# Kernel tuning notes

Hardware: AMD Instinct MI355X
Metric: run time of the kernel (lower is better)

## Reference

```python
import jax, jax.numpy as jnp
import numpy as np

N_NODES = 100000
N_EDGES = 1600000
N_GRAPHS = 64
N_TYPES = 17   # len(TYPES)
D = 128        # embedding_dim == hidden_dim
H = 128
O = 128


def setup_inputs() -> dict:
    key = jax.random.key(0)
    ks = jax.random.split(key, 8)
    node_ids = jax.random.randint(ks[0], (N_NODES,), 0, N_TYPES)
    edge_index = jax.random.randint(ks[1], (2, N_EDGES), 0, N_NODES)
    batch = jnp.sort(jax.random.randint(ks[2], (N_NODES,), 0, N_GRAPHS))
    emb_table = jax.random.normal(ks[3], (N_TYPES, D), dtype=jnp.float32)
    W1 = jax.random.normal(ks[4], (D, H), dtype=jnp.float32) * (1.0 / np.sqrt(D))
    b1 = jnp.zeros((H,), dtype=jnp.float32)
    W2 = jax.random.normal(ks[5], (H, O), dtype=jnp.float32) * (1.0 / np.sqrt(H))
    b2 = jnp.zeros((O,), dtype=jnp.float32)
    return {"node_ids": node_ids, "edge_index": edge_index, "batch": batch,
            "num_graphs": N_GRAPHS, "emb_table": emb_table,
            "W1": W1, "b1": b1, "W2": W2, "b2": b2}


def _gcn_conv(x, W, b, src, dst, n_nodes):
    # PyG GCNConv: h = x W; symmetric norm with self-loops (src/dst already include them);
    # out[i] = sum_{e: dst_e=i} norm_e * h[src_e] + b
    h = x @ W
    deg = jax.ops.segment_sum(jnp.ones_like(dst, dtype=h.dtype), dst,
                              num_segments=n_nodes)
    dinv = jnp.where(deg > 0, jax.lax.rsqrt(deg), 0.0)
    norm = dinv[src] * dinv[dst]                      # [E+N]
    msgs = h[src] * norm[:, None]                     # [E+N, out_dim]
    return jax.ops.segment_sum(msgs, dst, num_segments=n_nodes) + b


def reference(node_ids, edge_index, batch, num_graphs, emb_table, W1, b1, W2, b2):
    n = node_ids.shape[0]
    loops = jnp.arange(n, dtype=edge_index.dtype)
    src = jnp.concatenate([edge_index[0], loops])
    dst = jnp.concatenate([edge_index[1], loops])

    x = emb_table[node_ids]                            # embedding lookup [N, D]
    x = _gcn_conv(x, W1, b1, src, dst, n)
    x = jax.nn.relu(x)
    # F.dropout(training=self.training) is identity in eval mode
    x = _gcn_conv(x, W2, b2, src, dst, n)

    # global_mean_pool over batch index
    sums = jax.ops.segment_sum(x, batch, num_segments=num_graphs)   # [G, O]
    cnts = jax.ops.segment_sum(jnp.ones((n,), dtype=x.dtype), batch,
                               num_segments=num_graphs)
    return sums / jnp.maximum(cnts, 1.0)[:, None]
```

## Files before the change

### kernel.cpp

```cpp
#include <hip/hip_runtime.h>
#include <hip/hip_bf16.h>


#define DDIM 128
#define GMAX 64
#define BPG  8
#define NBK  (GMAX * BPG)
#define BKCAP 4096
#define CHUNK 2048
#define MAXGN 2048
typedef unsigned int uint;
typedef unsigned short ushort;
typedef float v2f __attribute__((ext_vector_type(2)));

__global__ void __launch_bounds__(256) k_setup(
        const int* __restrict__ batch, int N,
        int* __restrict__ gBound, int* __restrict__ bkBound,
        const float* __restrict__ emb, const float* __restrict__ W1,
        float* __restrict__ t1) {
    int t = threadIdx.x, b = blockIdx.x;
    if (b == 0) {
        __shared__ int gB[GMAX + 1];
        if (t <= GMAX) {
            int key = t, lo = 0, hi = N;
            while (lo < hi) {
                int mid = (lo + hi) >> 1;
                if (batch[mid] < key) lo = mid + 1; else hi = mid;
            }
            gB[t] = lo;
            gBound[t] = lo;
        }
        __syncthreads();
        for (int bk = t; bk <= NBK; bk += 256) {
            int v;
            if (bk == NBK) v = gB[GMAX];
            else {
                int g = bk >> 3, s = bk & 7;
                int A = gB[g], L = gB[g + 1] - A;
                v = A + (int)(((long long)L * s + 7) / 8);
            }
            bkBound[bk] = v;
        }
    } else {
        int row = b - 1;
        if (t < DDIM) {
            float acc = 0.f;
            for (int k = 0; k < DDIM; k++) acc += emb[row * DDIM + k] * W1[k * DDIM + t];
            t1[row * DDIM + t] = acc;
        }
    }
}

__global__ void __launch_bounds__(256) k_ninfo(
        const int* __restrict__ batch, const int* __restrict__ gBound,
        uint* __restrict__ nodeInfo, int N) {
    int n = blockIdx.x * 256 + threadIdx.x;
    if (n >= N) return;
    int g = batch[n];
    int A = gBound[g], L = gBound[g + 1] - A;
    int o = n - A;
    int s = (8 * o) / L;
    nodeInfo[n] = ((uint)(g * BPG + s) << 12) | (uint)o;
}

__global__ void __launch_bounds__(256) k_partA(
        const int* __restrict__ src, const int* __restrict__ dst,
        const uint* __restrict__ nodeInfo, int* __restrict__ bkCnt,
        uint* __restrict__ partsKey, int E) {
    __shared__ int rk[NBK];
    __shared__ int runOff[NBK];
    __shared__ int base[NBK];
    __shared__ int sms[256];
    __shared__ uint sbuf[CHUNK];
    __shared__ ushort sb2[CHUNK];
    int t = threadIdx.x, b = blockIdx.x;
    int lo = b * CHUNK;
    int hi = lo + CHUNK; if (hi > E) hi = E;
    int cnt = hi - lo;
    for (int k = t; k < NBK; k += 256) rk[k] = 0;
    __syncthreads();
    uint key_[8]; int bk_[8], r_[8]; bool v_[8];
    if (cnt == CHUNK) {
        int4 sA = *(const int4*)(src + lo + t * 4);
        int4 sB = *(const int4*)(src + lo + 1024 + t * 4);
        int4 dA = *(const int4*)(dst + lo + t * 4);
        int4 dB = *(const int4*)(dst + lo + 1024 + t * 4);
        int ss[8] = {sA.x, sA.y, sA.z, sA.w, sB.x, sB.y, sB.z, sB.w};
        int dd[8] = {dA.x, dA.y, dA.z, dA.w, dB.x, dB.y, dB.z, dB.w};
#pragma unroll
        for (int q = 0; q < 8; q++) {
            v_[q] = true;
            uint info = nodeInfo[dd[q]];
            bk_[q] = (int)(info >> 12);
            key_[q] = ((info & 0xFFFu) << 17) | (uint)ss[q];
        }
    } else {
#pragma unroll
        for (int q = 0; q < 8; q++) {
            int item = lo + q * 256 + t;
            v_[q] = item < hi;
            key_[q] = 0; bk_[q] = 0;
            if (v_[q]) {
                uint info = nodeInfo[dst[item]];
                bk_[q] = (int)(info >> 12);
                key_[q] = ((info & 0xFFFu) << 17) | (uint)src[item];
            }
        }
    }
#pragma unroll
    for (int q = 0; q < 8; q++)
        if (v_[q]) r_[q] = atomicAdd(&rk[bk_[q]], 1);
    __syncthreads();
    {
        int v0 = rk[2 * t], v1 = rk[2 * t + 1];
        int run = v0 + v1;
        sms[t] = run; __syncthreads();
        for (int off = 1; off < 256; off <<= 1) {
            int a = (t >= off) ? sms[t - off] : 0;
            __syncthreads();
            sms[t] += a; __syncthreads();
        }
        int excl = sms[t] - run;
        runOff[2 * t] = excl;
        runOff[2 * t + 1] = excl + v0;
    }
    __syncthreads();
    for (int k = t; k < NBK; k += 256) {
        int c = rk[k];
        if (c > 0) base[k] = k * BKCAP + atomicAdd(&bkCnt[k], c);
    }
#pragma unroll
    for (int q = 0; q < 8; q++)
        if (v_[q]) {
            int p = runOff[bk_[q]] + r_[q];
            sbuf[p] = key_[q];
            sb2[p] = (ushort)bk_[q];
        }
    __syncthreads();
#pragma unroll
    for (int q = 0; q < 8; q++) {
        int p = q * 256 + t;
        if (p < cnt) {
            int bk = sb2[p];
            partsKey[base[bk] + (p - runOff[bk])] = sbuf[p];
        }
    }
}

__global__ void __launch_bounds__(256) k_cnt2(
        const uint* __restrict__ partsKey, const int* __restrict__ bkBound,
        const int* __restrict__ bkCnt, const int* __restrict__ ids,
        float2* __restrict__ nd, float* __restrict__ dinvA) {
    __shared__ int cnt[256];
    int b = blockIdx.x, t = threadIdx.x;
    cnt[t] = 0;
    __syncthreads();
    int nodeLo = bkBound[b];
    int gOff = nodeLo - bkBound[(b >> 3) << 3];
    int lo = b * BKCAP, hi = lo + bkCnt[b];
    for (int idx = lo + t; idx < hi; idx += 256) {
        uint key = partsKey[idx];
        int dL = (int)((key >> 17) & 0xFFF) - gOff;
        atomicAdd(&cnt[dL], 1);
    }
    __syncthreads();
    int nn = bkBound[b + 1] - nodeLo;
    if (t < nn) {
        int i = nodeLo + t;
        float dinv = rsqrtf((float)(cnt[t] + 1));
        nd[i] = make_float2(dinv, __int_as_float(ids[i]));
        dinvA[i] = dinv;
    }
}

__global__ void __launch_bounds__(256) k_x1b(
        const uint* __restrict__ partsKey, const int* __restrict__ bkBound,
        const int* __restrict__ bkCnt, const float2* __restrict__ nd,
        const float* __restrict__ t1, const float* __restrict__ b1,
        ushort* __restrict__ z, float* __restrict__ poolY) {
    __shared__ float t1s[17 * DDIM];
    __shared__ float CL[256 * 17];
    __shared__ float2 ndL[256];
    __shared__ float bL[DDIM];
    __shared__ float redS[4][DDIM];
    int b = blockIdx.x, t = threadIdx.x;
    int nodeLo = bkBound[b], nn = bkBound[b + 1] - nodeLo;
    int gOff = nodeLo - bkBound[(b >> 3) << 3];
    for (int k = t; k < 17 * DDIM; k += 256) t1s[k] = t1[k];
    for (int k = t; k < 256 * 17; k += 256) CL[k] = 0.f;
    if (t < DDIM) bL[t] = b1[t];
    if (t < nn) ndL[t] = nd[nodeLo + t];
    __syncthreads();
    int lo = b * BKCAP, hi = lo + bkCnt[b];
    for (int cb = lo; cb < hi; cb += 2048) {
        uint key_[8]; bool v_[8];
#pragma unroll
        for (int q = 0; q < 8; q++) {
            int idx = cb + q * 256 + t;
            v_[q] = idx < hi;
            key_[q] = v_[q] ? partsKey[idx] : 0u;
        }
#pragma unroll
        for (int q = 0; q < 8; q++) {
            if (v_[q]) {
                uint key = key_[q];
                int s = key & 0x1FFFF;
                int dL = (int)((key >> 17) & 0xFFF) - gOff;
                float2 ns = nd[s];
                atomicAdd(&CL[dL * 17 + __float_as_int(ns.y)], ns.x);
            }
        }
    }
    __syncthreads();
    int lane = t & 63, wave = t >> 6;
    float sx = 0.f, sy = 0.f;
    for (int n = wave; n < nn; n += 4) {
        float dinv = ndL[n].x;
        int ti = __float_as_int(ndL[n].y);
        float ax = dinv * t1s[ti * DDIM + lane];
        float ay = dinv * t1s[ti * DDIM + 64 + lane];
#pragma unroll
        for (int tt = 0; tt < 17; tt++) {
            float c = CL[n * 17 + tt];
            ax += c * t1s[tt * DDIM + lane];
            ay += c * t1s[tt * DDIM + 64 + lane];
        }
        float vx = bL[lane]      + dinv * ax;
        float vy = bL[64 + lane] + dinv * ay;
        vx = vx > 0.f ? vx : 0.f;
        vy = vy > 0.f ? vy : 0.f;
        int pk = __builtin_amdgcn_cvt_pk_fp8_f32(dinv * vx, dinv * vy, 0, false);
        z[(size_t)(nodeLo + n) * 64 + lane] = (ushort)(pk & 0xFFFF);
        float d2 = dinv * dinv;
        sx += d2 * vx;
        sy += d2 * vy;
    }
    redS[wave][lane] = sx;
    redS[wave][64 + lane] = sy;
    __syncthreads();
    if (wave == 0) {
        int g = b >> 3;
        float vx = redS[0][lane] + redS[1][lane] + redS[2][lane] + redS[3][lane];
        float vy = redS[0][64 + lane] + redS[1][64 + lane]
                 + redS[2][64 + lane] + redS[3][64 + lane];
        atomicAdd(&poolY[g * DDIM + lane], vx);
        atomicAdd(&poolY[g * DDIM + 64 + lane], vy);
    }
}

__global__ void __launch_bounds__(256) k_conv2g(
        const uint* __restrict__ partsKey, const int* __restrict__ bkCnt,
        const int* __restrict__ gBound, const float* __restrict__ dinvA,
        const ushort* __restrict__ z, float* __restrict__ poolY) {
    __shared__ float dinvG[MAXGN];
    __shared__ uint  mk[4][64];
    __shared__ float red[4][DDIM];
    int t = threadIdx.x, lane = t & 63, wave = t >> 6;
    int b = blockIdx.x;
    int j = b >> 3;
    int g = (b & 7) * 8 + (j >> 5);
    int r = j & 31;
    int bk = g * BPG + (r >> 2);
    int q = r & 3;
    int nLo = gBound[g], nn = gBound[g + 1] - nLo;
    for (int k = t; k < nn; k += 256) dinvG[k] = dinvA[nLo + k];
    if (t == 0) dinvG[MAXGN - 1] = 0.f;
    __syncthreads();
    int c = bkCnt[bk];
    int base0 = bk * BKCAP;
    int s0 = base0 + (c * q) / 4;
    int s1 = base0 + (c * (q + 1)) / 4;
    const uint SENT = (uint)(MAXGN - 1) << 17;
    float ax = 0.f, ay = 0.f;
    for (int cb = s0 + wave * 64; cb < s1; cb += 4 * 64) {
        int idx = cb + lane;
        mk[wave][lane] = (idx < s1) ? partsKey[idx] : SENT;
#pragma unroll
        for (int jj = 0; jj < 64; jj += 16) {
            uint kk[16]; uint vv[16];
#pragma unroll
            for (int k = 0; k < 16; k++) kk[k] = mk[wave][jj + k];
#pragma unroll
            for (int k = 0; k < 16; k++)
                vv[k] = (uint)z[(size_t)(kk[k] & 0x1FFFF) * 64 + lane];
#pragma unroll
            for (int k = 0; k < 16; k++) {
                float w = dinvG[(kk[k] >> 17) & 0xFFF];
                v2f f = __builtin_amdgcn_cvt_pk_f32_fp8((int)vv[k], false);
                ax += w * f.x;
                ay += w * f.y;
            }
        }
    }
    red[wave][lane] = ax;
    red[wave][64 + lane] = ay;
    __syncthreads();
    if (wave == 0) {
        float vx = red[0][lane] + red[1][lane] + red[2][lane] + red[3][lane];
        float vy = red[0][64 + lane] + red[1][64 + lane] + red[2][64 + lane] + red[3][64 + lane];
        atomicAdd(&poolY[g * DDIM + lane], vx);
        atomicAdd(&poolY[g * DDIM + 64 + lane], vy);
    }
}

__global__ void __launch_bounds__(128) k_out(
        const float* __restrict__ poolY, const int* __restrict__ gBound,
        const float* __restrict__ W2, const float* __restrict__ b2,
        float* __restrict__ out) {
    __shared__ float py[DDIM];
    int g = blockIdx.x, f = threadIdx.x;
    py[f] = poolY[g * DDIM + f];
    __syncthreads();
    float acc = 0.f;
    for (int k = 0; k < DDIM; k++) acc += py[k] * W2[k * DDIM + f];
    int c = gBound[g + 1] - gBound[g];
    out[g * DDIM + f] = (c > 0) ? (b2[f] + acc / (float)c) : 0.f;
}

extern "C" void kernel_launch(void* const* d_in, const int* in_sizes, int n_in,
                              void* d_out, int out_size, void* d_ws, size_t ws_size,
                              hipStream_t stream) {
    const int* node_ids = (const int*)d_in[0];
    const int* edge_index = (const int*)d_in[1];
    const int* batch = (const int*)d_in[2];
    const float* emb = (const float*)d_in[4];
    const float* W1 = (const float*)d_in[5];
    const float* b1 = (const float*)d_in[6];
    const float* W2 = (const float*)d_in[7];
    const float* b2 = (const float*)d_in[8];
    float* out = (float*)d_out;

    const int N = in_sizes[0];
    const int E = in_sizes[1] / 2;
    const int* src = edge_index;
    const int* dst = edge_index + E;

    char* ws = (char*)d_ws;
    size_t off = 0;
    auto carve = [&](size_t bytes) { char* p = ws + off; off = (off + bytes + 255) & ~size_t(255); return p; };
    ushort* z        = (ushort*)carve((size_t)N * 64 * 2);
    uint*   partsKey = (uint*)carve((size_t)NBK * BKCAP * 4);
    float2* nd       = (float2*)carve((size_t)N * 8);
    float*  dinvA    = (float*)carve((size_t)N * 4);
    uint*   nodeInfo = (uint*)carve((size_t)N * 4);
    int*    gBound   = (int*)carve((GMAX + 1) * 4);
    int*    bkBound  = (int*)carve((NBK + 1) * 4);
    float*  t1       = (float*)carve(17 * DDIM * 4);
    float*  poolY    = (float*)carve((size_t)GMAX * DDIM * 4);
    int*    bkCnt    = (int*)carve(NBK * 4);

    hipMemsetAsync(poolY, 0, (size_t)GMAX * DDIM * 4 + NBK * 4, stream);

    int nblkE = (E + CHUNK - 1) / CHUNK;
    int nblkN = (N + 255) / 256;

    k_setup<<<18, 256, 0, stream>>>(batch, N, gBound, bkBound, emb, W1, t1);
    k_ninfo<<<nblkN, 256, 0, stream>>>(batch, gBound, nodeInfo, N);
    k_partA<<<nblkE, 256, 0, stream>>>(src, dst, nodeInfo, bkCnt, partsKey, E);
    k_cnt2<<<NBK, 256, 0, stream>>>(partsKey, bkBound, bkCnt, node_ids, nd, dinvA);
    k_x1b<<<NBK, 256, 0, stream>>>(partsKey, bkBound, bkCnt, nd, t1, b1, z, poolY);
    k_conv2g<<<GMAX * 32, 256, 0, stream>>>(partsKey, bkCnt, gBound,
                                            dinvA, z, poolY);
    k_out<<<GMAX, 128, 0, stream>>>(poolY, gBound, W2, b2, out);
}
```

Measured before the change: 185.5 us.

## Fold degree counting into partition pass and merge setup kernels

Removes the separate degree-count kernel. In-degree is now accumulated with global atomics in the edge-partition kernel into a packed per-node word that holds degree<<5 | type id. Consumers recompute rsqrt(deg+1) from that word instead of reading precomputed dinv arrays. The node-info computation and the zeroing of the pool and bucket counters move into the setup kernel, which drops one memset and one launch. The cost is 1.6M global atomics and two binary searches per node.

```diff
diff --git a/kernel.cpp b/kernel.cpp
--- a/kernel.cpp
+++ b/kernel.cpp
@@ -13,60 +13,64 @@
 typedef unsigned short ushort;
 typedef float v2f __attribute__((ext_vector_type(2)));
 
+__device__ __forceinline__ int lbound(const int* a, int n, int key) {
+    int lo = 0, hi = n;
+    while (lo < hi) { int mid = (lo + hi) >> 1; if (a[mid] < key) lo = mid + 1; else hi = mid; }
+    return lo;
+}
+
 __global__ void __launch_bounds__(256) k_setup(
-        const int* __restrict__ batch, int N,
+        const int* __restrict__ batch, const int* __restrict__ ids, int N,
         int* __restrict__ gBound, int* __restrict__ bkBound,
         const float* __restrict__ emb, const float* __restrict__ W1,
-        float* __restrict__ t1) {
+        float* __restrict__ t1, uint* __restrict__ nodeInfo,
+        uint* __restrict__ pdt, float* __restrict__ poolY,
+        int* __restrict__ bkCnt) {
     int t = threadIdx.x, b = blockIdx.x;
     if (b == 0) {
         __shared__ int gB[GMAX + 1];
-        if (t <= GMAX) {
-            int key = t, lo = 0, hi = N;
-            while (lo < hi) {
-                int mid = (lo + hi) >> 1;
-                if (batch[mid] < key) lo = mid + 1; else hi = mid;
-            }
-            gB[t] = lo;
-            gBound[t] = lo;
-        }
+        if (t <= GMAX) { int lo = lbound(batch, N, t); gB[t] = lo; gBound[t] = lo; }
         __syncthreads();
         for (int bk = t; bk <= NBK; bk += 256) {
             int v;
             if (bk == NBK) v = gB[GMAX];
             else {
                 int g = bk >> 3, s = bk & 7;
-                int A = gB[g], L = gB[g + 1] - A;
-                v = A + (int)(((long long)L * s + 7) / 8);
+                int A0 = gB[g], L = gB[g + 1] - A0;
+                v = A0 + (int)(((long long)L * s + 7) / 8);
             }
             bkBound[bk] = v;
         }
-    } else {
+        return;
+    }
+    if (b <= 17) {
         int row = b - 1;
         if (t < DDIM) {
             float acc = 0.f;
-            for (int k = 0; k < DDIM; k++) acc += emb[row * DDIM + k] * W1[k * DDIM + t];
+            for (int k = 0; k < DDIM; k++)
+                acc += emb[row * DDIM + k] * W1[k * DDIM + t];
             t1[row * DDIM + t] = acc;
         }
-    }
-}
-
-__global__ void __launch_bounds__(256) k_ninfo(
-        const int* __restrict__ batch, const int* __restrict__ gBound,
-        uint* __restrict__ nodeInfo, int N) {
-    int n = blockIdx.x * 256 + threadIdx.x;
-    if (n >= N) return;
-    int g = batch[n];
-    int A = gBound[g], L = gBound[g + 1] - A;
-    int o = n - A;
-    int s = (8 * o) / L;
-    nodeInfo[n] = ((uint)(g * BPG + s) << 12) | (uint)o;
+        return;
+    }
+    int idx = (b - 18) * 256 + t;
+    if (idx < GMAX * DDIM) poolY[idx] = 0.f;
+    if (idx < NBK) bkCnt[idx] = 0;
+    if (idx < N) {
+        int g = batch[idx];
+        int A0 = lbound(batch, N, g);
+        int A1 = lbound(batch, N, g + 1);
+        int o = idx - A0;
+        int s = (8 * o) / (A1 - A0);
+        nodeInfo[idx] = ((uint)(g * BPG + s) << 12) | (uint)o;
+        pdt[idx] = (uint)ids[idx];
+    }
 }
 
 __global__ void __launch_bounds__(256) k_partA(
         const int* __restrict__ src, const int* __restrict__ dst,
         const uint* __restrict__ nodeInfo, int* __restrict__ bkCnt,
-        uint* __restrict__ partsKey, int E) {
+        uint* __restrict__ partsKey, uint* __restrict__ pdt, int E) {
     __shared__ int rk[NBK];
     __shared__ int runOff[NBK];
     __shared__ int base[NBK];
@@ -93,6 +97,7 @@
             uint info = nodeInfo[dd[q]];
             bk_[q] = (int)(info >> 12);
             key_[q] = ((info & 0xFFFu) << 17) | (uint)ss[q];
+            atomicAdd(&pdt[dd[q]], 32u);
         }
     } else {
 #pragma unroll
@@ -101,9 +106,11 @@
             v_[q] = item < hi;
             key_[q] = 0; bk_[q] = 0;
             if (v_[q]) {
-                uint info = nodeInfo[dst[item]];
+                int d = dst[item];
+                uint info = nodeInfo[d];
                 bk_[q] = (int)(info >> 12);
                 key_[q] = ((info & 0xFFFu) << 17) | (uint)src[item];
+                atomicAdd(&pdt[d], 32u);
             }
         }
     }
@@ -147,35 +154,9 @@
     }
 }
 
-__global__ void __launch_bounds__(256) k_cnt2(
-        const uint* __restrict__ partsKey, const int* __restrict__ bkBound,
-        const int* __restrict__ bkCnt, const int* __restrict__ ids,
-        float2* __restrict__ nd, float* __restrict__ dinvA) {
-    __shared__ int cnt[256];
-    int b = blockIdx.x, t = threadIdx.x;
-    cnt[t] = 0;
-    __syncthreads();
-    int nodeLo = bkBound[b];
-    int gOff = nodeLo - bkBound[(b >> 3) << 3];
-    int lo = b * BKCAP, hi = lo + bkCnt[b];
-    for (int idx = lo + t; idx < hi; idx += 256) {
-        uint key = partsKey[idx];
-        int dL = (int)((key >> 17) & 0xFFF) - gOff;
-        atomicAdd(&cnt[dL], 1);
-    }
-    __syncthreads();
-    int nn = bkBound[b + 1] - nodeLo;
-    if (t < nn) {
-        int i = nodeLo + t;
-        float dinv = rsqrtf((float)(cnt[t] + 1));
-        nd[i] = make_float2(dinv, __int_as_float(ids[i]));
-        dinvA[i] = dinv;
-    }
-}
-
 __global__ void __launch_bounds__(256) k_x1b(
         const uint* __restrict__ partsKey, const int* __restrict__ bkBound,
-        const int* __restrict__ bkCnt, const float2* __restrict__ nd,
+        const int* __restrict__ bkCnt, const uint* __restrict__ pdt,
         const float* __restrict__ t1, const float* __restrict__ b1,
         ushort* __restrict__ z, float* __restrict__ poolY) {
     __shared__ float t1s[17 * DDIM];
@@ -189,11 +170,15 @@
     for (int k = t; k < 17 * DDIM; k += 256) t1s[k] = t1[k];
     for (int k = t; k < 256 * 17; k += 256) CL[k] = 0.f;
     if (t < DDIM) bL[t] = b1[t];
-    if (t < nn) ndL[t] = nd[nodeLo + t];
+    if (t < nn) {
+        uint p = pdt[nodeLo + t];
+        ndL[t] = make_float2(rsqrtf((float)(p >> 5) + 1.f),
+                             __int_as_float((int)(p & 31u)));
+    }
     __syncthreads();
     int lo = b * BKCAP, hi = lo + bkCnt[b];
     for (int cb = lo; cb < hi; cb += 2048) {
-        uint key_[8]; bool v_[8];
+        uint key_[8], pp_[8]; bool v_[8];
 #pragma unroll
         for (int q = 0; q < 8; q++) {
             int idx = cb + q * 256 + t;
@@ -201,13 +186,15 @@
             key_[q] = v_[q] ? partsKey[idx] : 0u;
         }
 #pragma unroll
+        for (int q = 0; q < 8; q++)
+            if (v_[q]) pp_[q] = pdt[key_[q] & 0x1FFFF];
+#pragma unroll
         for (int q = 0; q < 8; q++) {
             if (v_[q]) {
-                uint key = key_[q];
-                int s = key & 0x1FFFF;
-                int dL = (int)((key >> 17) & 0xFFF) - gOff;
-                float2 ns = nd[s];
-                atomicAdd(&CL[dL * 17 + __float_as_int(ns.y)], ns.x);
+                int dL = (int)((key_[q] >> 17) & 0xFFF) - gOff;
+                uint p = pp_[q];
+                float dv = rsqrtf((float)(p >> 5) + 1.f);
+                atomicAdd(&CL[dL * 17 + (int)(p & 31u)], dv);
             }
         }
     }
@@ -250,7 +237,7 @@
 
 __global__ void __launch_bounds__(256) k_conv2g(
         const uint* __restrict__ partsKey, const int* __restrict__ bkCnt,
-        const int* __restrict__ gBound, const float* __restrict__ dinvA,
+        const int* __restrict__ gBound, const uint* __restrict__ pdt,
         const ushort* __restrict__ z, float* __restrict__ poolY) {
     __shared__ float dinvG[MAXGN];
     __shared__ uint  mk[4][64];
@@ -263,7 +250,8 @@
     int bk = g * BPG + (r >> 2);
     int q = r & 3;
     int nLo = gBound[g], nn = gBound[g + 1] - nLo;
-    for (int k = t; k < nn; k += 256) dinvG[k] = dinvA[nLo + k];
+    for (int k = t; k < nn; k += 256)
+        dinvG[k] = rsqrtf((float)(pdt[nLo + k] >> 5) + 1.f);
     if (t == 0) dinvG[MAXGN - 1] = 0.f;
     __syncthreads();
     int c = bkCnt[bk];
@@ -340,26 +328,23 @@
     auto carve = [&](size_t bytes) { char* p = ws + off; off = (off + bytes + 255) & ~size_t(255); return p; };
     ushort* z        = (ushort*)carve((size_t)N * 64 * 2);
     uint*   partsKey = (uint*)carve((size_t)NBK * BKCAP * 4);
-    float2* nd       = (float2*)carve((size_t)N * 8);
-    float*  dinvA    = (float*)carve((size_t)N * 4);
     uint*   nodeInfo = (uint*)carve((size_t)N * 4);
+    uint*   pdt      = (uint*)carve((size_t)N * 4);
     int*    gBound   = (int*)carve((GMAX + 1) * 4);
     int*    bkBound  = (int*)carve((NBK + 1) * 4);
     float*  t1       = (float*)carve(17 * DDIM * 4);
     float*  poolY    = (float*)carve((size_t)GMAX * DDIM * 4);
     int*    bkCnt    = (int*)carve(NBK * 4);
 
-    hipMemsetAsync(poolY, 0, (size_t)GMAX * DDIM * 4 + NBK * 4, stream);
-
     int nblkE = (E + CHUNK - 1) / CHUNK;
-    int nblkN = (N + 255) / 256;
-
-    k_setup<<<18, 256, 0, stream>>>(batch, N, gBound, bkBound, emb, W1, t1);
-    k_ninfo<<<nblkN, 256, 0, stream>>>(batch, gBound, nodeInfo, N);
-    k_partA<<<nblkE, 256, 0, stream>>>(src, dst, nodeInfo, bkCnt, partsKey, E);
-    k_cnt2<<<NBK, 256, 0, stream>>>(partsKey, bkBound, bkCnt, node_ids, nd, dinvA);
-    k_x1b<<<NBK, 256, 0, stream>>>(partsKey, bkBound, bkCnt, nd, t1, b1, z, poolY);
+    int nblkS = 18 + (N + 255) / 256;
+
+    k_setup<<<nblkS, 256, 0, stream>>>(batch, node_ids, N, gBound, bkBound,
+                                       emb, W1, t1, nodeInfo, pdt, poolY, bkCnt);
+    k_partA<<<nblkE, 256, 0, stream>>>(src, dst, nodeInfo, bkCnt, partsKey,
+                                       pdt, E);
+    k_x1b<<<NBK, 256, 0, stream>>>(partsKey, bkBound, bkCnt, pdt, t1, b1, z, poolY);
     k_conv2g<<<GMAX * 32, 256, 0, stream>>>(partsKey, bkCnt, gBound,
-                                            dinvA, z, poolY);
+                                            pdt, z, poolY);
     k_out<<<GMAX, 128, 0, stream>>>(poolY, gBound, W2, b2, out);
 }
```

After: 239.2 us. +28.9%, slower.
